# Kernel optimization log

Hardware: AMD Instinct MI355X
Metric: run time of the kernel (lower is better)

The kernel has to match this reference:

```python
import jax, jax.numpy as jnp
import numpy as np

B, S, H = 128, 2048, 512


def setup_inputs() -> dict:
    key = jax.random.key(0)
    ks = jax.random.split(key, 8)
    s = 1.0 / np.sqrt(H)
    return {
        "query": jax.random.normal(ks[0], (B, 1, H), jnp.float32),
        "keys": jax.random.normal(ks[1], (B, S, H), jnp.float32),
        "Wa": jax.random.uniform(ks[2], (H, H), jnp.float32, -s, s),
        "ba": jax.random.uniform(ks[3], (H,), jnp.float32, -s, s),
        "Ua": jax.random.uniform(ks[4], (H, H), jnp.float32, -s, s),
        "bu": jax.random.uniform(ks[5], (H,), jnp.float32, -s, s),
        "Va": jax.random.uniform(ks[6], (1, H), jnp.float32, -s, s),
        "bv": jax.random.uniform(ks[7], (1,), jnp.float32, -s, s),
    }


def reference(query, keys, Wa, ba, Ua, bu, Va, bv):
    # Wa(query): [B,1,H]; Ua(keys): [B,S,H]
    wq = jnp.einsum('bqh,oh->bqo', query, Wa) + ba
    uk = jnp.einsum('bsh,oh->bso', keys, Ua) + bu
    # additive score: Va(tanh(wq + uk)) -> [B,S,1] -> [B,1,S]
    t = jnp.tanh(wq + uk)                      # [B,S,H]
    scores = jnp.einsum('bsh,oh->bso', t, Va) + bv  # [B,S,1]
    scores = jnp.swapaxes(scores, 1, 2)        # [B,1,S]
    weights = jax.nn.softmax(scores, axis=-1)  # [B,1,S]
    context = jnp.einsum('bqs,bsh->bqh', weights, keys)  # [B,1,H]
    return context, weights
```

## Files before the change

kernel.cpp:

```cpp
#include <hip/hip_runtime.h>


#define BM 128
#define BN 128
#define BK 32
#define LDK 40

typedef __attribute__((ext_vector_type(8))) short bf16x8;
typedef __attribute__((ext_vector_type(4))) float f32x4;

static __device__ inline short f2bf(float f) {
  unsigned u = __float_as_uint(f);
  unsigned r = (u + 0x7FFFu + ((u >> 16) & 1u)) >> 16;
  return (short)r;
}

static __device__ inline void store8(short* dst, float4 a, float4 b) {
  union { bf16x8 v; short s[8]; } u;
  u.s[0] = f2bf(a.x); u.s[1] = f2bf(a.y); u.s[2] = f2bf(a.z); u.s[3] = f2bf(a.w);
  u.s[4] = f2bf(b.x); u.s[5] = f2bf(b.y); u.s[6] = f2bf(b.z); u.s[7] = f2bf(b.w);
  *(bf16x8*)dst = u.v;
}

__global__ __launch_bounds__(512) void wq_kernel(const float* __restrict__ query,
                                                 const float* __restrict__ Wa,
                                                 const float* __restrict__ ba,
                                                 const float* __restrict__ bu,
                                                 float* __restrict__ wqb) {
  const int b = blockIdx.x;
  const int o = threadIdx.x;
  __shared__ float qs[512];
  qs[o] = query[(b << 9) + o];
  __syncthreads();
  const float4* w4 = (const float4*)(Wa + (size_t)o * 512);
  float acc = 0.f;
#pragma unroll 4
  for (int h = 0; h < 128; ++h) {
    float4 w = w4[h];
    acc += w.x * qs[4 * h] + w.y * qs[4 * h + 1] + w.z * qs[4 * h + 2] + w.w * qs[4 * h + 3];
  }
  wqb[(b << 9) + o] = acc + ba[o] + bu[o];
}

__global__ __launch_bounds__(256) void score_gemm(const float* __restrict__ keys,
                                                  const float* __restrict__ Ua,
                                                  const float* __restrict__ wqb,
                                                  const float* __restrict__ Va,
                                                  float* __restrict__ scores) {
  __shared__ short As[BM][LDK];
  __shared__ short Bs[BN][LDK];

  const int n0 = blockIdx.x * BN;
  const int m0 = blockIdx.y * BM;
  const int b = m0 >> 11;

  const int tid = threadIdx.x;
  const int lane = tid & 63;
  const int wave = tid >> 6;
  const int wm = (wave >> 1) * 64;
  const int wn = (wave & 1) * 64;
  const int mlane = lane & 15;
  const int quad = lane >> 4;

  const int sr = tid >> 2;
  const int sc = (tid & 3) * 8;

  f32x4 zero = {0.f, 0.f, 0.f, 0.f};
  f32x4 acc[4][4];
#pragma unroll
  for (int i = 0; i < 4; ++i)
#pragma unroll
    for (int j = 0; j < 4; ++j) acc[i][j] = zero;

  for (int k0 = 0; k0 < 512; k0 += BK) {
    __syncthreads();
#pragma unroll
    for (int it = 0; it < 2; ++it) {
      const int row = sr + it * 64;
      const float* pa = keys + (size_t)(m0 + row) * 512 + k0 + sc;
      const float* pb = Ua + (size_t)(n0 + row) * 512 + k0 + sc;
      float4 a0 = *(const float4*)pa;
      float4 a1 = *(const float4*)(pa + 4);
      float4 b0 = *(const float4*)pb;
      float4 b1 = *(const float4*)(pb + 4);
      store8(&As[row][sc], a0, a1);
      store8(&Bs[row][sc], b0, b1);
    }
    __syncthreads();

    bf16x8 af[4], bfr[4];
#pragma unroll
    for (int i = 0; i < 4; ++i) af[i] = *(const bf16x8*)&As[wm + i * 16 + mlane][quad * 8];
#pragma unroll
    for (int j = 0; j < 4; ++j) bfr[j] = *(const bf16x8*)&Bs[wn + j * 16 + mlane][quad * 8];
#pragma unroll
    for (int i = 0; i < 4; ++i)
#pragma unroll
      for (int j = 0; j < 4; ++j)
        acc[i][j] = __builtin_amdgcn_mfma_f32_16x16x32_bf16(af[i], bfr[j], acc[i][j], 0, 0, 0);
  }

  float wqv[4], vav[4];
#pragma unroll
  for (int j = 0; j < 4; ++j) {
    const int n = n0 + wn + j * 16 + mlane;
    wqv[j] = wqb[(b << 9) + n];
    vav[j] = Va[n];
  }
  float rs[4][4] = {};
#pragma unroll
  for (int j = 0; j < 4; ++j)
#pragma unroll
    for (int i = 0; i < 4; ++i)
#pragma unroll
      for (int r = 0; r < 4; ++r) {
        const float v = acc[i][j][r] + wqv[j];
        const float e = __expf(2.0f * v);
        const float t = 1.0f - 2.0f * __builtin_amdgcn_rcpf(e + 1.0f);
        rs[i][r] += vav[j] * t;
      }
#pragma unroll
  for (int i = 0; i < 4; ++i)
#pragma unroll
    for (int r = 0; r < 4; ++r) {
      float v = rs[i][r];
      v += __shfl_xor(v, 1);
      v += __shfl_xor(v, 2);
      v += __shfl_xor(v, 4);
      v += __shfl_xor(v, 8);
      if (mlane == 0) {
        const int m = m0 + wm + i * 16 + quad * 4 + r;
        atomicAdd(&scores[m], v);
      }
    }
}

__global__ __launch_bounds__(256) void softmax_kernel(float* __restrict__ sw,
                                                      float* __restrict__ context) {
  const int b = blockIdx.x;
  const int t = threadIdx.x;
  context[(b << 9) + t] = 0.f;
  context[(b << 9) + 256 + t] = 0.f;

  float* row = sw + (size_t)(b << 11);
  float4 x0 = *(float4*)(row + t * 8);
  float4 x1 = *(float4*)(row + t * 8 + 4);

  float mx = fmaxf(fmaxf(fmaxf(x0.x, x0.y), fmaxf(x0.z, x0.w)),
                   fmaxf(fmaxf(x1.x, x1.y), fmaxf(x1.z, x1.w)));
#pragma unroll
  for (int d = 1; d < 64; d <<= 1) mx = fmaxf(mx, __shfl_xor(mx, d));

  __shared__ float smax[4], ssum[4];
  const int wave = t >> 6, lane = t & 63;
  if (lane == 0) smax[wave] = mx;
  __syncthreads();
  mx = fmaxf(fmaxf(smax[0], smax[1]), fmaxf(smax[2], smax[3]));

  float e[8];
  e[0] = __expf(x0.x - mx); e[1] = __expf(x0.y - mx);
  e[2] = __expf(x0.z - mx); e[3] = __expf(x0.w - mx);
  e[4] = __expf(x1.x - mx); e[5] = __expf(x1.y - mx);
  e[6] = __expf(x1.z - mx); e[7] = __expf(x1.w - mx);
  float s = e[0] + e[1] + e[2] + e[3] + e[4] + e[5] + e[6] + e[7];
#pragma unroll
  for (int d = 1; d < 64; d <<= 1) s += __shfl_xor(s, d);
  if (lane == 0) ssum[wave] = s;
  __syncthreads();
  s = ssum[0] + ssum[1] + ssum[2] + ssum[3];
  const float inv = 1.0f / s;

  float4 y0, y1;
  y0.x = e[0] * inv; y0.y = e[1] * inv; y0.z = e[2] * inv; y0.w = e[3] * inv;
  y1.x = e[4] * inv; y1.y = e[5] * inv; y1.z = e[6] * inv; y1.w = e[7] * inv;
  *(float4*)(row + t * 8) = y0;
  *(float4*)(row + t * 8 + 4) = y1;
}

__global__ __launch_bounds__(256) void context_kernel(const float* __restrict__ keys,
                                                      const float* __restrict__ weights,
                                                      float* __restrict__ context) {
  const int b = blockIdx.x >> 2;
  const int chunk = blockIdx.x & 3;
  const int t = threadIdx.x;
  const int hg = t & 63;
  const int sl = t >> 6;

  float acc[8] = {0.f, 0.f, 0.f, 0.f, 0.f, 0.f, 0.f, 0.f};
  const float* wrow = weights + (size_t)(b << 11) + (chunk << 9);
  const float* kbase = keys + ((size_t)(b << 11) + (chunk << 9)) * 512 + hg * 8;
  for (int s = sl; s < 512; s += 4) {
    const float w = wrow[s];
    const float* kp = kbase + (size_t)s * 512;
    float4 k0 = *(const float4*)kp;
    float4 k1 = *(const float4*)(kp + 4);
    acc[0] += w * k0.x; acc[1] += w * k0.y; acc[2] += w * k0.z; acc[3] += w * k0.w;
    acc[4] += w * k1.x; acc[5] += w * k1.y; acc[6] += w * k1.z; acc[7] += w * k1.w;
  }
  __shared__ float red[4][512];
  float4 r0, r1;
  r0.x = acc[0]; r0.y = acc[1]; r0.z = acc[2]; r0.w = acc[3];
  r1.x = acc[4]; r1.y = acc[5]; r1.z = acc[6]; r1.w = acc[7];
  *(float4*)&red[sl][hg * 8] = r0;
  *(float4*)&red[sl][hg * 8 + 4] = r1;
  __syncthreads();
#pragma unroll
  for (int hh = 0; hh < 2; ++hh) {
    const int h = t + hh * 256;
    const float v = red[0][h] + red[1][h] + red[2][h] + red[3][h];
    atomicAdd(&context[(b << 9) + h], v);
  }
}

extern "C" void kernel_launch(void* const* d_in, const int* in_sizes, int n_in,
                              void* d_out, int out_size, void* d_ws, size_t ws_size,
                              hipStream_t stream) {
  const float* query = (const float*)d_in[0];
  const float* keys  = (const float*)d_in[1];
  const float* Wa    = (const float*)d_in[2];
  const float* ba    = (const float*)d_in[3];
  const float* Ua    = (const float*)d_in[4];
  const float* bu    = (const float*)d_in[5];
  const float* Va    = (const float*)d_in[6];

  float* out = (float*)d_out;
  float* context = out;
  float* weights = out + 65536;
  float* wqb = context;

  hipMemsetAsync(weights, 0, (size_t)262144 * sizeof(float), stream);

  wq_kernel<<<dim3(128), dim3(512), 0, stream>>>(query, Wa, ba, bu, wqb);

  dim3 g2(4, 2048);
  score_gemm<<<g2, dim3(256), 0, stream>>>(keys, Ua, wqb, Va, weights);

  softmax_kernel<<<dim3(128), dim3(256), 0, stream>>>(weights, context);

  context_kernel<<<dim3(512), dim3(256), 0, stream>>>(keys, weights, context);
}
```

Baseline: 1.022 ms.

## Pre-convert keys and Ua to bf16 in workspace and use async LDS loads

Adds a conversion pass that writes keys and Ua as bf16 into the workspace, then runs a bf16 score GEMM that fills LDS with global_load_lds async copies, using a remapped block order so the four N-tiles of one M-tile run close together. The context kernel also reads the bf16 keys, halving the bytes it streams but lowering its precision. The conversion pass adds a full read of keys plus a half-size write, so the total traffic may not fall; the old path is kept as a fallback when the workspace is too small.

```diff
diff --git a/kernel.cpp b/kernel.cpp
--- a/kernel.cpp
+++ b/kernel.cpp
@@ -1,10 +1,8 @@
 #include <hip/hip_runtime.h>
 
 
-#define BM 128
-#define BN 128
-#define BK 32
-#define LDK 40
+#define KEYS_N 134217728ull
+#define UA_N   262144ull
 
 typedef __attribute__((ext_vector_type(8))) short bf16x8;
 typedef __attribute__((ext_vector_type(4))) float f32x4;
@@ -20,6 +18,19 @@
   u.s[0] = f2bf(a.x); u.s[1] = f2bf(a.y); u.s[2] = f2bf(a.z); u.s[3] = f2bf(a.w);
   u.s[4] = f2bf(b.x); u.s[5] = f2bf(b.y); u.s[6] = f2bf(b.z); u.s[7] = f2bf(b.w);
   *(bf16x8*)dst = u.v;
+}
+
+static __device__ inline void async16(const void* g, void* l) {
+  __builtin_amdgcn_global_load_lds((const __attribute__((address_space(1))) void*)g,
+                                   (__attribute__((address_space(3))) void*)l, 16, 0, 0);
+}
+
+__global__ __launch_bounds__(256) void convert_kernel(const float* __restrict__ in,
+                                                      short* __restrict__ out) {
+  const size_t i = ((size_t)blockIdx.x * 256 + threadIdx.x) * 8;
+  const float4* p = (const float4*)(in + i);
+  float4 a = p[0], b = p[1];
+  store8(out + i, a, b);
 }
 
 __global__ __launch_bounds__(512) void wq_kernel(const float* __restrict__ query,
@@ -42,16 +53,18 @@
   wqb[(b << 9) + o] = acc + ba[o] + bu[o];
 }
 
-__global__ __launch_bounds__(256) void score_gemm(const float* __restrict__ keys,
-                                                  const float* __restrict__ Ua,
-                                                  const float* __restrict__ wqb,
-                                                  const float* __restrict__ Va,
-                                                  float* __restrict__ scores) {
-  __shared__ short As[BM][LDK];
-  __shared__ short Bs[BN][LDK];
-
-  const int n0 = blockIdx.x * BN;
-  const int m0 = blockIdx.y * BM;
+__global__ __launch_bounds__(256) void score_gemm_bf16(const short* __restrict__ keys,
+                                                       const short* __restrict__ ua,
+                                                       const float* __restrict__ wqb,
+                                                       const float* __restrict__ Va,
+                                                       float* __restrict__ scores) {
+  __shared__ short As[128][32];
+  __shared__ short Bs[128][32];
+
+  const int id = blockIdx.x;
+  const int s = id >> 3;
+  const int m0 = ((id & 7) * 256 + (s >> 2)) * 128;
+  const int n0 = (s & 3) * 128;
   const int b = m0 >> 11;
 
   const int tid = threadIdx.x;
@@ -62,6 +75,89 @@
   const int mlane = lane & 15;
   const int quad = lane >> 4;
 
+  const int lrow = lane >> 2;
+  const int lcol = (lane & 3) * 8;
+
+  f32x4 acc[4][4];
+  f32x4 zero = {0.f, 0.f, 0.f, 0.f};
+#pragma unroll
+  for (int i = 0; i < 4; ++i)
+#pragma unroll
+    for (int j = 0; j < 4; ++j) acc[i][j] = zero;
+
+  const short* gA = keys + (size_t)(m0 + wave * 32 + lrow) * 512 + lcol;
+  const short* gB = ua + (size_t)(n0 + wave * 32 + lrow) * 512 + lcol;
+
+  for (int k0 = 0; k0 < 512; k0 += 32) {
+    __syncthreads();
+    async16(gA + k0, &As[wave * 32][0]);
+    async16(gA + k0 + 16 * 512, &As[wave * 32 + 16][0]);
+    async16(gB + k0, &Bs[wave * 32][0]);
+    async16(gB + k0 + 16 * 512, &Bs[wave * 32 + 16][0]);
+    __syncthreads();
+
+    bf16x8 af[4], bfr[4];
+#pragma unroll
+    for (int i = 0; i < 4; ++i) af[i] = *(const bf16x8*)&As[wm + i * 16 + mlane][quad * 8];
+#pragma unroll
+    for (int j = 0; j < 4; ++j) bfr[j] = *(const bf16x8*)&Bs[wn + j * 16 + mlane][quad * 8];
+#pragma unroll
+    for (int i = 0; i < 4; ++i)
+#pragma unroll
+      for (int j = 0; j < 4; ++j)
+        acc[i][j] = __builtin_amdgcn_mfma_f32_16x16x32_bf16(af[i], bfr[j], acc[i][j], 0, 0, 0);
+  }
+
+  float wqv[4], vav[4];
+#pragma unroll
+  for (int j = 0; j < 4; ++j) {
+    const int n = n0 + wn + j * 16 + mlane;
+    wqv[j] = wqb[(b << 9) + n];
+    vav[j] = Va[n];
+  }
+  float rs[4][4] = {};
+#pragma unroll
+  for (int j = 0; j < 4; ++j)
+#pragma unroll
+    for (int i = 0; i < 4; ++i)
+#pragma unroll
+      for (int r = 0; r < 4; ++r) {
+        const float v = acc[i][j][r] + wqv[j];
+        const float e = __expf(2.0f * v);
+        const float t = 1.0f - 2.0f * __builtin_amdgcn_rcpf(e + 1.0f);
+        rs[i][r] += vav[j] * t;
+      }
+#pragma unroll
+  for (int i = 0; i < 4; ++i)
+#pragma unroll
+    for (int r = 0; r < 4; ++r) {
+      float v = rs[i][r];
+      v += __shfl_xor(v, 1);
+      v += __shfl_xor(v, 2);
+      v += __shfl_xor(v, 4);
+      v += __shfl_xor(v, 8);
+      if (mlane == 0) atomicAdd(&scores[m0 + wm + i * 16 + quad * 4 + r], v);
+    }
+}
+
+#define LDK 40
+__global__ __launch_bounds__(256) void score_gemm(const float* __restrict__ keys,
+                                                  const float* __restrict__ Ua,
+                                                  const float* __restrict__ wqb,
+                                                  const float* __restrict__ Va,
+                                                  float* __restrict__ scores) {
+  __shared__ short As[128][LDK];
+  __shared__ short Bs[128][LDK];
+  const int n0 = blockIdx.x * 128;
+  const int m0 = blockIdx.y * 128;
+  const int b = m0 >> 11;
+  const int tid = threadIdx.x;
+  const int lane = tid & 63;
+  const int wave = tid >> 6;
+  const int wm = (wave >> 1) * 64;
+  const int wn = (wave & 1) * 64;
+  const int mlane = lane & 15;
+  const int quad = lane >> 4;
   const int sr = tid >> 2;
   const int sc = (tid & 3) * 8;
 
@@ -72,7 +168,7 @@
 #pragma unroll
     for (int j = 0; j < 4; ++j) acc[i][j] = zero;
 
-  for (int k0 = 0; k0 < 512; k0 += BK) {
+  for (int k0 = 0; k0 < 512; k0 += 32) {
     __syncthreads();
 #pragma unroll
     for (int it = 0; it < 2; ++it) {
@@ -87,7 +183,6 @@
       store8(&Bs[row][sc], b0, b1);
     }
     __syncthreads();
-
     bf16x8 af[4], bfr[4];
 #pragma unroll
     for (int i = 0; i < 4; ++i) af[i] = *(const bf16x8*)&As[wm + i * 16 + mlane][quad * 8];
@@ -99,7 +194,6 @@
       for (int j = 0; j < 4; ++j)
         acc[i][j] = __builtin_amdgcn_mfma_f32_16x16x32_bf16(af[i], bfr[j], acc[i][j], 0, 0, 0);
   }
-
   float wqv[4], vav[4];
 #pragma unroll
   for (int j = 0; j < 4; ++j) {
@@ -128,10 +222,7 @@
       v += __shfl_xor(v, 2);
       v += __shfl_xor(v, 4);
       v += __shfl_xor(v, 8);
-      if (mlane == 0) {
-        const int m = m0 + wm + i * 16 + quad * 4 + r;
-        atomicAdd(&scores[m], v);
-      }
+      if (mlane == 0) atomicAdd(&scores[m0 + wm + i * 16 + quad * 4 + r], v);
     }
 }
 
@@ -175,6 +266,41 @@
   y1.x = e[4] * inv; y1.y = e[5] * inv; y1.z = e[6] * inv; y1.w = e[7] * inv;
   *(float4*)(row + t * 8) = y0;
   *(float4*)(row + t * 8 + 4) = y1;
+}
+
+__global__ __launch_bounds__(256) void context_bf16(const short* __restrict__ keys,
+                                                    const float* __restrict__ weights,
+                                                    float* __restrict__ context) {
+  const int b = blockIdx.x >> 2;
+  const int chunk = blockIdx.x & 3;
+  const int t = threadIdx.x;
+  const int hg = t & 63;
+  const int sl = t >> 6;
+
+  float acc[8] = {0.f, 0.f, 0.f, 0.f, 0.f, 0.f, 0.f, 0.f};
+  const float* wrow = weights + (size_t)(b << 11) + (chunk << 9);
+  const short* kbase = keys + ((size_t)(b << 11) + (chunk << 9)) * 512 + hg * 8;
+  for (int s = sl; s < 512; s += 4) {
+    const float w = wrow[s];
+    union { bf16x8 v; unsigned short u[8]; } kv;
+    kv.v = *(const bf16x8*)(kbase + (size_t)s * 512);
+#pragma unroll
+    for (int j = 0; j < 8; ++j)
+      acc[j] += w * __uint_as_float(((unsigned)kv.u[j]) << 16);
+  }
+  __shared__ float red[4][512];
+  float4 r0, r1;
+  r0.x = acc[0]; r0.y = acc[1]; r0.z = acc[2]; r0.w = acc[3];
+  r1.x = acc[4]; r1.y = acc[5]; r1.z = acc[6]; r1.w = acc[7];
+  *(float4*)&red[sl][hg * 8] = r0;
+  *(float4*)&red[sl][hg * 8 + 4] = r1;
+  __syncthreads();
+#pragma unroll
+  for (int hh = 0; hh < 2; ++hh) {
+    const int h = t + hh * 256;
+    const float v = red[0][h] + red[1][h] + red[2][h] + red[3][h];
+    atomicAdd(&context[(b << 9) + h], v);
+  }
 }
 
 __global__ __launch_bounds__(256) void context_kernel(const float* __restrict__ keys,
@@ -185,7 +311,6 @@
   const int t = threadIdx.x;
   const int hg = t & 63;
   const int sl = t >> 6;
-
   float acc[8] = {0.f, 0.f, 0.f, 0.f, 0.f, 0.f, 0.f, 0.f};
   const float* wrow = weights + (size_t)(b << 11) + (chunk << 9);
   const float* kbase = keys + ((size_t)(b << 11) + (chunk << 9)) * 512 + hg * 8;
@@ -228,14 +353,26 @@
   float* weights = out + 65536;
   float* wqb = context;
 
+  const bool planA = ws_size >= (KEYS_N + UA_N) * sizeof(short);
+
   hipMemsetAsync(weights, 0, (size_t)262144 * sizeof(float), stream);
-
   wq_kernel<<<dim3(128), dim3(512), 0, stream>>>(query, Wa, ba, bu, wqb);
 
-  dim3 g2(4, 2048);
-  score_gemm<<<g2, dim3(256), 0, stream>>>(keys, Ua, wqb, Va, weights);
+  if (planA) {
+    short* kbf = (short*)d_ws;
+    short* ubf = kbf + KEYS_N;
+    convert_kernel<<<dim3(65536), dim3(256), 0, stream>>>(keys, kbf);
+    convert_kernel<<<dim3(128), dim3(256), 0, stream>>>(Ua, ubf);
+    score_gemm_bf16<<<dim3(8192), dim3(256), 0, stream>>>(kbf, ubf, wqb, Va, weights);
+  } else {
+    score_gemm<<<dim3(4, 2048), dim3(256), 0, stream>>>(keys, Ua, wqb, Va, weights);
+  }
 
   softmax_kernel<<<dim3(128), dim3(256), 0, stream>>>(weights, context);
 
-  context_kernel<<<dim3(512), dim3(256), 0, stream>>>(keys, weights, context);
-}
+  if (planA) {
+    context_bf16<<<dim3(512), dim3(256), 0, stream>>>((short*)d_ws, weights, context);
+  } else {
+    context_kernel<<<dim3(512), dim3(256), 0, stream>>>(keys, weights, context);
+  }
+}
```

New measurement: 1.034 ms. No clear change (+1.1%).
